# Kernel optimization log

Hardware: AMD Instinct MI355X
Metric: run time of the kernel (lower is better)

## Reference

```python
import jax, jax.numpy as jnp
import numpy as np

# Physical constants from Config
VT = 0.026
N_FACTOR = 1.5
VD = 0.2
ALPHA = 1e-05
TIA_GAIN = 2000.0
PHI = 2.0 * N_FACTOR * VT  # 0.078
K = 3  # kernel_size (hardcoded in DoubleEKVBlock)


def _unfold3x3(x):
    # x: (N, C, H, W) -> (N, C*9, H*W), matching torch F.unfold ordering
    # (channel-major, then kh, then kw), with padding=1, stride=1.
    N, C, H, W = x.shape
    xp = jnp.pad(x, ((0, 0), (0, 0), (1, 1), (1, 1)))
    cols = jnp.stack(
        [xp[:, :, i:i + H, j:j + W] for i in range(K) for j in range(K)],
        axis=2,
    )  # (N, C, 9, H, W)
    return cols.reshape(N, C * K * K, H * W)


def _ekv_conv(x, theta_pos, theta_neg):
    # Differential EKV 'convolution': elementwise softplus^2 nonlinearity on
    # (patch element - threshold), summed over the patch dim.
    N, C, H, W = x.shape
    O = theta_pos.shape[0]
    L = H * W
    x_in = _unfold3x3(x)[:, None]  # (N, 1, C*9, L)

    def current(theta):
        v_th = theta.reshape(1, O, C * K * K, 1)
        i_f = jax.nn.softplus((x_in - v_th) / PHI) ** 2
        i_r = jax.nn.softplus((x_in - v_th - VD) / PHI) ** 2
        return ALPHA * (i_f - i_r)

    # sum(i_pos) - sum(i_neg) == sum(i_pos - i_neg)
    i_diff = jnp.sum(current(theta_pos) - current(theta_neg), axis=2)  # (N, O, L)
    return (i_diff * TIA_GAIN).reshape(N, O, H, W)


def _voltage_mapper(x, scale, bias):
    real_scale = jnp.clip(jnp.abs(scale), 0.01, 3.0)
    return jnp.clip(x * real_scale + bias, 0.0, 8.0)


def setup_inputs() -> dict:
    key = jax.random.key(0)
    ks = jax.random.split(key, 5)
    N, C, H, W = 4, 32, 32, 32  # in_planes = planes = 32, stride = 1
    O = 32
    x = jax.random.normal(ks[0], (N, C, H, W), dtype=jnp.float32)
    # theta ~ Normal(4.0, 0.5)
    tp1 = 4.0 + 0.5 * jax.random.normal(ks[1], (O, C, K, K), dtype=jnp.float32)
    tn1 = 4.0 + 0.5 * jax.random.normal(ks[2], (O, C, K, K), dtype=jnp.float32)
    tp2 = 4.0 + 0.5 * jax.random.normal(ks[3], (O, O, K, K), dtype=jnp.float32)
    tn2 = 4.0 + 0.5 * jax.random.normal(ks[4], (O, O, K, K), dtype=jnp.float32)
    scale1 = jnp.ones((1, C, 1, 1), dtype=jnp.float32)
    bias1 = 4.0 * jnp.ones((1, C, 1, 1), dtype=jnp.float32)
    scale2 = jnp.ones((1, O, 1, 1), dtype=jnp.float32)
    bias2 = 4.0 * jnp.ones((1, O, 1, 1), dtype=jnp.float32)
    return {
        "x": x,
        "scale1": scale1, "bias1": bias1, "tp1": tp1, "tn1": tn1,
        "scale2": scale2, "bias2": bias2, "tp2": tp2, "tn2": tn2,
    }


def reference(x, scale1, bias1, tp1, tn1, scale2, bias2, tp2, tn2):
    # DoubleEKVBlock forward (eval mode: Dropout2d is identity; shortcut is
    # identity since stride==1 and in_planes==planes).
    identity = x
    out = _voltage_mapper(x, scale1, bias1)
    out = _ekv_conv(out, tp1, tn1)
    out = _voltage_mapper(out, scale2, bias2)
    out = _ekv_conv(out, tp2, tn2)
    return jax.nn.relu(out + identity)
```

## Files before the change

### kernel.cpp

```cpp
#include <hip/hip_runtime.h>
#include <cmath>


constexpr int Cc = 32, Oc = 32, Hc = 32, Wc = 32;
constexpr int OT = 4;
constexpr int WTILE = 16;
constexpr int TPB = 256;
constexpr int THS = 578;

template <int MODE>
__global__ __launch_bounds__(TPB, 8)
void ekv_pass(const float* __restrict__ vin,
              const float* __restrict__ thp,
              const float* __restrict__ thn,
              float* __restrict__ vout,
              const float* __restrict__ sc_in,
              const float* __restrict__ bi_in,
              const float* __restrict__ sc_out,
              const float* __restrict__ bi_out,
              const float* __restrict__ ident,
              float K1f, float EMS, float GAIN)
{
    __shared__ float thL[OT * THS];
    __shared__ float xv[3 * Cc * (WTILE + 2) + 4];
    __shared__ float red[4][64];

    const int t  = threadIdx.x;
    const int bx = blockIdx.x;
    const int ot = bx >> 1, wt = bx & 1;
    const int h  = blockIdx.y;
    const int n  = blockIdx.z;
    const int o0 = ot * OT;
    const int w0 = wt * WTILE;

    const float* tp_g = thp + o0 * 288;
    const float* tn_g = thn + o0 * 288;
#pragma unroll
    for (int k = 0; k < 5; ++k) {
        int idx = t + k * TPB;
        if (idx < OT * 288) {
            int ol = idx / 288, j = idx % 288;
            thL[ol * THS + 2 * j]     = __builtin_amdgcn_exp2f(fmaf(tp_g[idx], -K1f, 74.f));
            thL[ol * THS + 2 * j + 1] = __builtin_amdgcn_exp2f(fmaf(tn_g[idx], -K1f, 74.f));
        }
    }

#pragma unroll
    for (int k = 0; k < 7; ++k) {
        int idx = t + k * TPB;
        if (idx < 3 * Cc * (WTILE + 2)) {
            int dh = idx / (Cc * (WTILE + 2));
            int r  = idx % (Cc * (WTILE + 2));
            int c  = r / (WTILE + 2);
            int i  = r % (WTILE + 2);
            int hh = h + dh - 1;
            int ww = w0 + i - 1;
            float v = 0.f;
            if (hh >= 0 && hh < Hc && ww >= 0 && ww < Wc) {
                v = vin[((n * Cc + c) * Hc + hh) * Wc + ww];
                if (MODE == 0) {
                    float rs = fminf(fmaxf(fabsf(sc_in[c]), 0.01f), 3.0f);
                    v = fminf(fmaxf(fmaf(v, rs, bi_in[c]), 0.f), 8.f);
                }
            }
            xv[idx] = fmaf(v, K1f, -74.f);
        }
    }
    __syncthreads();

    const int ol = t & (OT - 1);
    const int s  = (t >> 2) & 15;
    const int cs = t >> 6;

    const float2* th2 = (const float2*)&thL[ol * THS];
    float acc1 = 0.f, acc2 = 0.f;
    for (int c = cs * 8; c < cs * 8 + 8; ++c) {
#pragma unroll
        for (int kh = 0; kh < 3; ++kh) {
            const float* xr = &xv[(kh * Cc + c) * (WTILE + 2) + s];
            const float2* tq = &th2[(c * 3 + kh) * 3];
#pragma unroll
            for (int kw = 0; kw < 3; ++kw) {
                float  E  = __builtin_amdgcn_exp2f(xr[kw]);
                float2 th = tq[kw];
                float ep  = E * th.x;
                float lap = __builtin_amdgcn_logf(1.f + ep);
                float lbp = __builtin_amdgcn_logf(fmaf(ep, EMS, 1.f));
                acc1 = fmaf(lap, lap, acc1);
                acc2 = fmaf(lbp, lbp, acc2);
                float en  = E * th.y;
                float lan = __builtin_amdgcn_logf(1.f + en);
                float lbn = __builtin_amdgcn_logf(fmaf(en, EMS, 1.f));
                acc2 = fmaf(lan, lan, acc2);
                acc1 = fmaf(lbn, lbn, acc1);
            }
        }
    }
    red[cs][t & 63] = acc1 - acc2;
    __syncthreads();

    if (t < 64) {
        float y = (red[0][t] + red[1][t] + red[2][t] + red[3][t]) * GAIN;
        const int eol = t & (OT - 1);
        const int es  = t >> 2;
        const int w = w0 + es;
        const int o = o0 + eol;
        const int oidx = ((n * Oc + o) * Hc + h) * Wc + w;
        if (MODE == 0) {
            float rs = fminf(fmaxf(fabsf(sc_out[o]), 0.01f), 3.0f);
            vout[oidx] = fminf(fmaxf(fmaf(y, rs, bi_out[o]), 0.f), 8.f);
        } else {
            vout[oidx] = fmaxf(y + ident[oidx], 0.f);
        }
    }
}

extern "C" void kernel_launch(void* const* d_in, const int* in_sizes, int n_in,
                              void* d_out, int out_size, void* d_ws, size_t ws_size,
                              hipStream_t stream) {
    const float* x      = (const float*)d_in[0];
    const float* scale1 = (const float*)d_in[1];
    const float* bias1  = (const float*)d_in[2];
    const float* tp1    = (const float*)d_in[3];
    const float* tn1    = (const float*)d_in[4];
    const float* scale2 = (const float*)d_in[5];
    const float* bias2  = (const float*)d_in[6];
    const float* tp2    = (const float*)d_in[7];
    const float* tn2    = (const float*)d_in[8];
    float* out = (float*)d_out;
    float* v2  = (float*)d_ws;

    const double PHI  = 2.0 * 1.5 * 0.026;
    const float  K1f  = (float)(1.4426950408889634 / PHI);
    const float  EMS  = (float)exp(-0.2 / PHI);
    const float  GAIN = (float)(0.02 * 0.6931471805599453 * 0.6931471805599453);

    dim3 grid(16, Hc, 4), block(TPB);
    ekv_pass<0><<<grid, block, 0, stream>>>(x,  tp1, tn1, v2,  scale1, bias1, scale2, bias2, nullptr,
                                            K1f, EMS, GAIN);
    ekv_pass<1><<<grid, block, 0, stream>>>(v2, tp2, tn2, out, nullptr, nullptr, nullptr, nullptr, x,
                                            K1f, EMS, GAIN);
}
```

Measured before the change: 115.8 us.

## Retile EKV kernel to full-width rows with two outputs per block

```diff
diff --git a/kernel.cpp b/kernel.cpp
--- a/kernel.cpp
+++ b/kernel.cpp
@@ -3,10 +3,10 @@
 
 
 constexpr int Cc = 32, Oc = 32, Hc = 32, Wc = 32;
-constexpr int OT = 4;
-constexpr int WTILE = 16;
+constexpr int OT = 2;
 constexpr int TPB = 256;
 constexpr int THS = 578;
+constexpr int XROW = 34;
 
 template <int MODE>
 __global__ __launch_bounds__(TPB, 8)
@@ -22,54 +22,59 @@
               float K1f, float EMS, float GAIN)
 {
     __shared__ float thL[OT * THS];
-    __shared__ float xv[3 * Cc * (WTILE + 2) + 4];
+    __shared__ float xv[3 * Cc * XROW + 4];
     __shared__ float red[4][64];
 
     const int t  = threadIdx.x;
-    const int bx = blockIdx.x;
-    const int ot = bx >> 1, wt = bx & 1;
+    const int ot = blockIdx.x;
     const int h  = blockIdx.y;
     const int n  = blockIdx.z;
     const int o0 = ot * OT;
-    const int w0 = wt * WTILE;
 
-    const float* tp_g = thp + o0 * 288;
-    const float* tn_g = thn + o0 * 288;
+    {
+        const int ol = t >> 7;
+        const float* tp_g = thp + (o0 + ol) * 288;
+        const float* tn_g = thn + (o0 + ol) * 288;
+        float* dst = &thL[ol * THS];
 #pragma unroll
-    for (int k = 0; k < 5; ++k) {
-        int idx = t + k * TPB;
-        if (idx < OT * 288) {
-            int ol = idx / 288, j = idx % 288;
-            thL[ol * THS + 2 * j]     = __builtin_amdgcn_exp2f(fmaf(tp_g[idx], -K1f, 74.f));
-            thL[ol * THS + 2 * j + 1] = __builtin_amdgcn_exp2f(fmaf(tn_g[idx], -K1f, 74.f));
+        for (int k = 0; k < 3; ++k) {
+            int j = (t & 127) + 128 * k;
+            if (j < 288) {
+                dst[2 * j]     = __builtin_amdgcn_exp2f(fmaf(tp_g[j], -K1f, 74.f));
+                dst[2 * j + 1] = __builtin_amdgcn_exp2f(fmaf(tn_g[j], -K1f, 74.f));
+            }
         }
     }
 
+    {
+        const int w = t & 31;
 #pragma unroll
-    for (int k = 0; k < 7; ++k) {
-        int idx = t + k * TPB;
-        if (idx < 3 * Cc * (WTILE + 2)) {
-            int dh = idx / (Cc * (WTILE + 2));
-            int r  = idx % (Cc * (WTILE + 2));
-            int c  = r / (WTILE + 2);
-            int i  = r % (WTILE + 2);
-            int hh = h + dh - 1;
-            int ww = w0 + i - 1;
+        for (int k = 0; k < 12; ++k) {
+            int row = (t >> 5) + 8 * k;
+            int dh  = row >> 5;
+            int c   = row & 31;
+            int hh  = h + dh - 1;
             float v = 0.f;
-            if (hh >= 0 && hh < Hc && ww >= 0 && ww < Wc) {
-                v = vin[((n * Cc + c) * Hc + hh) * Wc + ww];
+            if (hh >= 0 && hh < Hc) {
+                v = vin[((n * Cc + c) * Hc + hh) * Wc + w];
                 if (MODE == 0) {
                     float rs = fminf(fmaxf(fabsf(sc_in[c]), 0.01f), 3.0f);
                     v = fminf(fmaxf(fmaf(v, rs, bi_in[c]), 0.f), 8.f);
                 }
             }
-            xv[idx] = fmaf(v, K1f, -74.f);
+            xv[row * XROW + 1 + w] = fmaf(v, K1f, -74.f);
+        }
+        if (t < 192) {
+            int row  = t >> 1;
+            int side = t & 1;
+            xv[row * XROW + (side ? 33 : 0)] = -74.f;
         }
     }
     __syncthreads();
 
-    const int ol = t & (OT - 1);
-    const int s  = (t >> 2) & 15;
+    const int l  = t & 63;
+    const int w  = l & 31;
+    const int ol = l >> 5;
     const int cs = t >> 6;
 
     const float2* th2 = (const float2*)&thL[ol * THS];
@@ -77,7 +82,7 @@
     for (int c = cs * 8; c < cs * 8 + 8; ++c) {
 #pragma unroll
         for (int kh = 0; kh < 3; ++kh) {
-            const float* xr = &xv[(kh * Cc + c) * (WTILE + 2) + s];
+            const float* xr = &xv[(kh * Cc + c) * XROW + w];
             const float2* tq = &th2[(c * 3 + kh) * 3];
 #pragma unroll
             for (int kw = 0; kw < 3; ++kw) {
@@ -96,16 +101,14 @@
             }
         }
     }
-    red[cs][t & 63] = acc1 - acc2;
+    red[cs][l] = acc1 - acc2;
     __syncthreads();
 
     if (t < 64) {
         float y = (red[0][t] + red[1][t] + red[2][t] + red[3][t]) * GAIN;
-        const int eol = t & (OT - 1);
-        const int es  = t >> 2;
-        const int w = w0 + es;
-        const int o = o0 + eol;
-        const int oidx = ((n * Oc + o) * Hc + h) * Wc + w;
+        const int o  = o0 + (t >> 5);
+        const int ww = t & 31;
+        const int oidx = ((n * Oc + o) * Hc + h) * Wc + ww;
         if (MODE == 0) {
             float rs = fminf(fmaxf(fabsf(sc_out[o]), 0.01f), 3.0f);
             vout[oidx] = fminf(fmaxf(fmaf(y, rs, bi_out[o]), 0.f), 8.f);
```

Result: no change. 115.1 us (-0.7%).
